# Kernel tuning notes

Measured on AMD Instinct MI355X. Metric: run time of the kernel, lower is better.

The kernel has to match this reference:

```python
import jax, jax.numpy as jnp
import numpy as np

N_NODES = 50000
N_EDGES = 800000
IN_FEATS = 128
OUT_FEATS = 128


def setup_inputs() -> dict:
    key = jax.random.key(0)
    k1, k2, k3, k4 = jax.random.split(key, 4)
    feature = jax.random.normal(k1, (N_NODES, IN_FEATS), dtype=jnp.float32)
    src = jax.random.randint(k2, (N_EDGES,), 0, N_NODES, dtype=jnp.int64)
    dst = jax.random.randint(k3, (N_EDGES,), 0, N_NODES, dtype=jnp.int64)
    # nn.Linear(in_feats, out_feats): W is [out, in], b is [out]
    bound = 1.0 / np.sqrt(IN_FEATS)
    W = jax.random.uniform(k4, (OUT_FEATS, IN_FEATS), minval=-bound, maxval=bound, dtype=jnp.float32)
    b = jnp.zeros((OUT_FEATS,), dtype=jnp.float32)
    return {"feature": feature, "src": src, "dst": dst, "W": W, "b": b}


def reference(feature, src, dst, W, b):
    # DGL update_all(copy_src('h'), sum('m','h')): h'[v] = sum over edges u->v of h[u]
    n_nodes = feature.shape[0]
    msgs = feature[src]  # [E, in_feats] gather
    agg = jax.ops.segment_sum(msgs, dst, num_segments=n_nodes)  # [N, in_feats]
    # linear: agg @ W.T + b
    return jnp.einsum("ni,oi->no", agg, W) + b
```

## Files before the change

kernel.cpp:

```cpp
#include <hip/hip_runtime.h>
#include <hip/hip_bf16.h>

#define N_FEATS 128
#define SCAN_CHUNK 1024

typedef __attribute__((ext_vector_type(8))) short bf16x8;
typedef __attribute__((ext_vector_type(4))) float f32x4;

__device__ __forceinline__ unsigned short f32_to_bf16_rne(float f) {
    unsigned u = __float_as_uint(f);
    u = u + 0x7FFFu + ((u >> 16) & 1u);
    return (unsigned short)(u >> 16);
}
__device__ __forceinline__ unsigned pack2(float a, float b) {
    return (unsigned)f32_to_bf16_rne(a) | ((unsigned)f32_to_bf16_rne(b) << 16);
}

__launch_bounds__(256)
__global__ void gcn_transform_mfma(const float* __restrict__ feat,
                                   const float* __restrict__ W,
                                   unsigned short* __restrict__ Y,
                                   int* __restrict__ deg, int n_nodes) {
    __shared__ unsigned short wlds[N_FEATS * N_FEATS];

    const int t = threadIdx.x;
    const long long gid = (long long)blockIdx.x * 256 + t;
    if (gid < n_nodes) deg[gid] = 0;

    {
        const int row = t >> 1;
        const int gbase = (t & 1) * 8;
        const float* wsrc = W + (size_t)row * N_FEATS + gbase * 8;
#pragma unroll
        for (int g = 0; g < 8; ++g) {
            float4 x0 = *reinterpret_cast<const float4*>(wsrc + g * 8);
            float4 x1 = *reinterpret_cast<const float4*>(wsrc + g * 8 + 4);
            uint4 q;
            q.x = pack2(x0.x, x0.y);
            q.y = pack2(x0.z, x0.w);
            q.z = pack2(x1.x, x1.y);
            q.w = pack2(x1.z, x1.w);
            int byte = row * 256 + (gbase + g) * 16;
            byte ^= (row & 7) << 4;
            *reinterpret_cast<uint4*>(reinterpret_cast<char*>(wlds) + byte) = q;
        }
    }
    __syncthreads();

    const int row0 = (blockIdx.x * 4 + (t >> 6)) * 16;
    if (row0 >= n_nodes) return;
    const int l = t & 63;
    const int lr = l & 15;
    const int kb = l >> 4;

    bf16x8 afrag[4] = {};
    if (row0 + lr < n_nodes) {
        const float* aptr = feat + (size_t)(row0 + lr) * N_FEATS + kb * 8;
#pragma unroll
        for (int kk = 0; kk < 4; ++kk) {
            float4 x0 = *reinterpret_cast<const float4*>(aptr + kk * 32);
            float4 x1 = *reinterpret_cast<const float4*>(aptr + kk * 32 + 4);
            bf16x8 af;
            af[0] = (short)f32_to_bf16_rne(x0.x);
            af[1] = (short)f32_to_bf16_rne(x0.y);
            af[2] = (short)f32_to_bf16_rne(x0.z);
            af[3] = (short)f32_to_bf16_rne(x0.w);
            af[4] = (short)f32_to_bf16_rne(x1.x);
            af[5] = (short)f32_to_bf16_rne(x1.y);
            af[6] = (short)f32_to_bf16_rne(x1.z);
            af[7] = (short)f32_to_bf16_rne(x1.w);
            afrag[kk] = af;
        }
    }

    f32x4 acc[8];
#pragma unroll
    for (int nt = 0; nt < 8; ++nt) acc[nt] = (f32x4){0.f, 0.f, 0.f, 0.f};

#pragma unroll
    for (int nt = 0; nt < 8; ++nt) {
        const int brow = nt * 16 + lr;
        const int swz = (brow & 7) << 4;
#pragma unroll
        for (int kk = 0; kk < 4; ++kk) {
            int byte = brow * 256 + (kk * 4 + kb) * 16;
            byte ^= swz;
            bf16x8 bfrag = *reinterpret_cast<const bf16x8*>(
                reinterpret_cast<const char*>(wlds) + byte);
            acc[nt] = __builtin_amdgcn_mfma_f32_16x16x32_bf16(afrag[kk], bfrag, acc[nt], 0, 0, 0);
        }
    }

#pragma unroll
    for (int nt = 0; nt < 8; ++nt) {
        const int col = nt * 16 + lr;
#pragma unroll
        for (int j = 0; j < 4; ++j) {
            const int r = row0 + kb * 4 + j;
            if (r < n_nodes)
                Y[(size_t)r * N_FEATS + col] = f32_to_bf16_rne(acc[nt][j]);
        }
    }
}

__global__ void gcn_hist_pos(const int* __restrict__ src, const int* __restrict__ dst,
                             int* __restrict__ deg, int* __restrict__ pos,
                             int n_edges, int n_nodes) {
    int e = blockIdx.x * blockDim.x + threadIdx.x;
    if (e >= n_edges) return;
    int d = dst[e];
    int s = src[e];
    if ((unsigned)d < (unsigned)n_nodes && (unsigned)s < (unsigned)n_nodes)
        pos[e] = atomicAdd(&deg[d], 1);
}

__launch_bounds__(256)
__global__ void gcn_scan(const int* __restrict__ deg, int* __restrict__ row_start,
                         int n, int nchunks) {
    const int t = threadIdx.x;
    const int b = blockIdx.x;
    const int base = b * SCAN_CHUNK;

    int v = 0;
    for (int j = t; j < base; j += 256) v += deg[j];
    for (int d = 1; d < 64; d <<= 1) v += __shfl_xor(v, d, 64);
    __shared__ int owsum[4];
    __shared__ int s_off;
    if ((t & 63) == 0) owsum[t >> 6] = v;
    __syncthreads();
    if (t == 0) s_off = owsum[0] + owsum[1] + owsum[2] + owsum[3];
    __syncthreads();
    const int chunk_off = s_off;

    const int idx0 = base + t * 4;
    int x[4];
#pragma unroll
    for (int k = 0; k < 4; ++k) {
        int idx = idx0 + k;
        x[k] = (idx < n) ? deg[idx] : 0;
    }
    const int tsum = x[0] + x[1] + x[2] + x[3];

    const int lane = t & 63, w = t >> 6;
    int inc = tsum;
    for (int d = 1; d < 64; d <<= 1) {
        int sv = __shfl_up(inc, d, 64);
        if (lane >= d) inc += sv;
    }
    __shared__ int wsum[4];
    if (lane == 63) wsum[w] = inc;
    __syncthreads();
    int woff = 0;
    for (int i = 0; i < w; ++i) woff += wsum[i];

    int run = chunk_off + woff + inc - tsum;
#pragma unroll
    for (int k = 0; k < 4; ++k) {
        int idx = idx0 + k;
        if (idx < n) row_start[idx] = run;
        run += x[k];
    }

    if (t == 0 && b == nchunks - 1)
        row_start[n] = chunk_off + wsum[0] + wsum[1] + wsum[2] + wsum[3];
}

__global__ void gcn_build_csr_pos(const int* __restrict__ src, const int* __restrict__ dst,
                                  const int* __restrict__ row_start, const int* __restrict__ pos,
                                  int* __restrict__ csr_src, int n_edges, int n_nodes) {
    int e = blockIdx.x * blockDim.x + threadIdx.x;
    if (e >= n_edges) return;
    int d = dst[e];
    int s = src[e];
    if ((unsigned)d >= (unsigned)n_nodes || (unsigned)s >= (unsigned)n_nodes) return;
    csr_src[row_start[d] + pos[e]] = s;
}

#define BACC(acc, v)                                              \
    do {                                                          \
        unsigned uu;                                              \
        uu = (v).x;                                               \
        acc[0] += __uint_as_float(uu << 16);                      \
        acc[1] += __uint_as_float(uu & 0xFFFF0000u);              \
        uu = (v).y;                                               \
        acc[2] += __uint_as_float(uu << 16);                      \
        acc[3] += __uint_as_float(uu & 0xFFFF0000u);              \
        uu = (v).z;                                               \
        acc[4] += __uint_as_float(uu << 16);                      \
        acc[5] += __uint_as_float(uu & 0xFFFF0000u);              \
        uu = (v).w;                                               \
        acc[6] += __uint_as_float(uu << 16);                      \
        acc[7] += __uint_as_float(uu & 0xFFFF0000u);              \
    } while (0)

__launch_bounds__(256)
__global__ void gcn_aggregate_half(const uint4* __restrict__ Y,
                                   const int* __restrict__ row_start,
                                   const int* __restrict__ csr_src,
                                   const float* __restrict__ bias,
                                   float* __restrict__ out, int n_nodes) {
    const int wid = blockIdx.x * 4 + (threadIdx.x >> 6);
    const int half = (wid >= n_nodes) ? 1 : 0;
    const int node = wid - half * n_nodes;
    if (node >= n_nodes) return;
    const int l = threadIdx.x & 63;
    const int g = l >> 3;
    const int ql = l & 7;
    const int beg = row_start[node];
    const int end = row_start[node + 1];
    const int coff = half * 8 + ql;

    float a0[8] = {0,0,0,0,0,0,0,0};
    float a1[8] = {0,0,0,0,0,0,0,0};

    int i = beg;
    for (; i + 16 <= end; i += 16) {
        int s0 = csr_src[i + g];
        int s1 = csr_src[i + 8 + g];
        uint4 v0 = Y[(size_t)s0 * 16 + coff];
        uint4 v1 = Y[(size_t)s1 * 16 + coff];
        BACC(a0, v0);
        BACC(a1, v1);
    }
    if (i + 8 <= end) {
        int s0 = csr_src[i + g];
        uint4 v0 = Y[(size_t)s0 * 16 + coff];
        BACC(a0, v0);
        i += 8;
    }
    int rem = end - i;
    if (g < rem) {
        int s0 = csr_src[i + g];
        uint4 v0 = Y[(size_t)s0 * 16 + coff];
        BACC(a0, v0);
    }

    float r[8];
#pragma unroll
    for (int k = 0; k < 8; ++k) {
        r[k] = a0[k] + a1[k];
        r[k] += __shfl_xor(r[k], 8, 64);
        r[k] += __shfl_xor(r[k], 16, 64);
        r[k] += __shfl_xor(r[k], 32, 64);
    }

    if (g == 0) {
        const int cbase = half * 64 + ql * 8;
        const float4 b0 = *reinterpret_cast<const float4*>(bias + cbase);
        const float4 b1 = *reinterpret_cast<const float4*>(bias + cbase + 4);
        float4* o4 = reinterpret_cast<float4*>(out + (size_t)node * N_FEATS + cbase);
        o4[0] = make_float4(r[0] + b0.x, r[1] + b0.y, r[2] + b0.z, r[3] + b0.w);
        o4[1] = make_float4(r[4] + b1.x, r[5] + b1.y, r[6] + b1.z, r[7] + b1.w);
    }
}

__global__ void gcn_init_c(const float* __restrict__ W, float* __restrict__ Wt) {
    int t = blockIdx.x * blockDim.x + threadIdx.x;
    if (t < N_FEATS * N_FEATS) {
        int o = t >> 7;
        int i = t & 127;
        Wt[i * N_FEATS + o] = W[o * N_FEATS + i];
    }
}

__global__ void gcn_scatter_add(const float* __restrict__ feat,
                                const int* __restrict__ src,
                                const int* __restrict__ dst,
                                float* __restrict__ agg,
                                int n_edges, int n_nodes) {
    long long tid = (long long)blockIdx.x * blockDim.x + threadIdx.x;
    int e = (int)(tid >> 5);
    if (e >= n_edges) return;
    int j = (int)(tid & 31);
    int s = src[e];
    int d = dst[e];
    if ((unsigned)s >= (unsigned)n_nodes || (unsigned)d >= (unsigned)n_nodes) return;
    const float4 v = *reinterpret_cast<const float4*>(feat + (size_t)s * N_FEATS + j * 4);
    float* p = agg + (size_t)d * N_FEATS + j * 4;
    atomicAdd(p + 0, v.x);
    atomicAdd(p + 1, v.y);
    atomicAdd(p + 2, v.z);
    atomicAdd(p + 3, v.w);
}

__launch_bounds__(256)
__global__ void gcn_gemm_inplace(float* __restrict__ out,
                                 const float* __restrict__ Wt,
                                 const float* __restrict__ b,
                                 int n_nodes) {
    __shared__ float a_lds[32 * N_FEATS];

    const int t = threadIdx.x;
    const int node0 = blockIdx.x * 32;
    const int rows = min(32, n_nodes - node0);

    float4* a4 = reinterpret_cast<float4*>(a_lds);
    const float4* out4 = reinterpret_cast<const float4*>(out + (size_t)node0 * N_FEATS);
    const int nflt4 = rows * (N_FEATS / 4);
    for (int idx = t; idx < nflt4; idx += 256) a4[idx] = out4[idx];
    __syncthreads();

    const int oq = t & 31;
    const int ng = t >> 5;

    const float4 bb = reinterpret_cast<const float4*>(b)[oq];
    float4 acc[4];
#pragma unroll
    for (int k = 0; k < 4; ++k) acc[k] = bb;

    const float4* Wt4 = reinterpret_cast<const float4*>(Wt);
#pragma unroll 4
    for (int i = 0; i < N_FEATS; ++i) {
        const float4 w = Wt4[i * 32 + oq];
#pragma unroll
        for (int k = 0; k < 4; ++k) {
            const float a = a_lds[(ng * 4 + k) * N_FEATS + i];
            acc[k].x += a * w.x;
            acc[k].y += a * w.y;
            acc[k].z += a * w.z;
            acc[k].w += a * w.w;
        }
    }

    __syncthreads();

#pragma unroll
    for (int k = 0; k < 4; ++k) {
        const int r = ng * 4 + k;
        if (r < rows) {
            reinterpret_cast<float4*>(out + (size_t)(node0 + r) * N_FEATS)[oq] = acc[k];
        }
    }
}

extern "C" void kernel_launch(void* const* d_in, const int* in_sizes, int n_in,
                              void* d_out, int out_size, void* d_ws, size_t ws_size,
                              hipStream_t stream) {
    const float* feature = (const float*)d_in[0];
    const int*   src     = (const int*)d_in[1];
    const int*   dst     = (const int*)d_in[2];
    const float* W       = (const float*)d_in[3];
    const float* b       = (const float*)d_in[4];
    float* out = (float*)d_out;

    const int n_nodes = in_sizes[0] / N_FEATS;
    const int n_edges = in_sizes[1];
    const int nchunks = (n_nodes + SCAN_CHUNK - 1) / SCAN_CHUNK;

    char* ws = (char*)d_ws;
    size_t off = 0;
    auto take = [&](size_t bytes) -> char* {
        char* p = ws + off;
        off = (off + bytes + 255) & ~(size_t)255;
        return p;
    };
    int* deg       = (int*)take((size_t)n_nodes * sizeof(int));
    int* row_start = (int*)take(((size_t)n_nodes + 1) * sizeof(int));
    int* csr_src   = (int*)take((size_t)n_edges * sizeof(int));
    unsigned short* Yb = (unsigned short*)take((size_t)n_nodes * N_FEATS * sizeof(unsigned short));
    int* pos       = (int*)take((size_t)n_edges * sizeof(int));
    const bool tierA2 = (off <= ws_size);

    if (tierA2) {
        gcn_transform_mfma<<<(n_nodes + 63) / 64, 256, 0, stream>>>(
            feature, W, Yb, deg, n_nodes);
        const int eblocks = (n_edges + 255) / 256;
        gcn_hist_pos<<<eblocks, 256, 0, stream>>>(src, dst, deg, pos, n_edges, n_nodes);
        gcn_scan<<<nchunks, 256, 0, stream>>>(deg, row_start, n_nodes, nchunks);
        gcn_build_csr_pos<<<eblocks, 256, 0, stream>>>(
            src, dst, row_start, pos, csr_src, n_edges, n_nodes);
        const int nwaves = 2 * n_nodes;
        gcn_aggregate_half<<<(nwaves + 3) / 4, 256, 0, stream>>>(
            reinterpret_cast<const uint4*>(Yb), row_start, csr_src, b, out, n_nodes);
    } else {
        float* Wt = (float*)d_ws;
        gcn_init_c<<<(N_FEATS * N_FEATS + 255) / 256, 256, 0, stream>>>(W, Wt);
        hipMemsetAsync(d_out, 0, (size_t)n_nodes * N_FEATS * sizeof(float), stream);
        long long total = (long long)n_edges * 32;
        gcn_scatter_add<<<(int)((total + 255) / 256), 256, 0, stream>>>(
            feature, src, dst, out, n_edges, n_nodes);
        gcn_gemm_inplace<<<(n_nodes + 31) / 32, 256, 0, stream>>>(out, Wt, b, n_nodes);
    }
}
```

Measured before the change: 137.8 us.

## Precompute bf16 W once and read from global; one wave per node aggregation

Adds a small init kernel that converts W to bf16 once and zeroes the degree array, so the MFMA transform kernel no longer restages a 32KB swizzled LDS copy of W in every block and instead reads B fragments straight from global memory (likely served from cache). The aggregation kernel changes from two waves per node, each handling half the features, to one wave per node covering all 128 features, with four edges processed per step and four accumulator sets. This removes redundant per-block W conversion and halves the number of row_start reads per node. In exchange it adds a kernel launch and relies on cache hits for the B reads, and the aggregation uses more registers per wave with less edge-level parallelism.

```diff
diff --git a/kernel.cpp b/kernel.cpp
--- a/kernel.cpp
+++ b/kernel.cpp
@@ -12,44 +12,36 @@
     u = u + 0x7FFFu + ((u >> 16) & 1u);
     return (unsigned short)(u >> 16);
 }
-__device__ __forceinline__ unsigned pack2(float a, float b) {
-    return (unsigned)f32_to_bf16_rne(a) | ((unsigned)f32_to_bf16_rne(b) << 16);
+
+__global__ void gcn_init(const float* __restrict__ W, unsigned short* __restrict__ Wb,
+                         int* __restrict__ deg, int n_nodes) {
+    int t = blockIdx.x * blockDim.x + threadIdx.x;
+    if (t < N_FEATS * N_FEATS / 8) {
+        const float4* f4 = reinterpret_cast<const float4*>(W) + (size_t)t * 2;
+        float4 x0 = f4[0];
+        float4 x1 = f4[1];
+        ushort4 o0, o1;
+        o0.x = f32_to_bf16_rne(x0.x); o0.y = f32_to_bf16_rne(x0.y);
+        o0.z = f32_to_bf16_rne(x0.z); o0.w = f32_to_bf16_rne(x0.w);
+        o1.x = f32_to_bf16_rne(x1.x); o1.y = f32_to_bf16_rne(x1.y);
+        o1.z = f32_to_bf16_rne(x1.z); o1.w = f32_to_bf16_rne(x1.w);
+        reinterpret_cast<ushort4*>(Wb)[(size_t)t * 2 + 0] = o0;
+        reinterpret_cast<ushort4*>(Wb)[(size_t)t * 2 + 1] = o1;
+    }
+    int u = t - N_FEATS * N_FEATS / 8;
+    if (u >= 0 && u < n_nodes) deg[u] = 0;
 }
 
 __launch_bounds__(256)
 __global__ void gcn_transform_mfma(const float* __restrict__ feat,
-                                   const float* __restrict__ W,
+                                   const unsigned short* __restrict__ Wb,
                                    unsigned short* __restrict__ Y,
-                                   int* __restrict__ deg, int n_nodes) {
-    __shared__ unsigned short wlds[N_FEATS * N_FEATS];
-
-    const int t = threadIdx.x;
-    const long long gid = (long long)blockIdx.x * 256 + t;
-    if (gid < n_nodes) deg[gid] = 0;
-
-    {
-        const int row = t >> 1;
-        const int gbase = (t & 1) * 8;
-        const float* wsrc = W + (size_t)row * N_FEATS + gbase * 8;
-#pragma unroll
-        for (int g = 0; g < 8; ++g) {
-            float4 x0 = *reinterpret_cast<const float4*>(wsrc + g * 8);
-            float4 x1 = *reinterpret_cast<const float4*>(wsrc + g * 8 + 4);
-            uint4 q;
-            q.x = pack2(x0.x, x0.y);
-            q.y = pack2(x0.z, x0.w);
-            q.z = pack2(x1.x, x1.y);
-            q.w = pack2(x1.z, x1.w);
-            int byte = row * 256 + (gbase + g) * 16;
-            byte ^= (row & 7) << 4;
-            *reinterpret_cast<uint4*>(reinterpret_cast<char*>(wlds) + byte) = q;
-        }
-    }
-    __syncthreads();
-
-    const int row0 = (blockIdx.x * 4 + (t >> 6)) * 16;
+                                   int n_nodes) {
+    const long long gtid = (long long)blockIdx.x * blockDim.x + threadIdx.x;
+    const int wave = (int)(gtid >> 6);
+    const int row0 = wave * 16;
     if (row0 >= n_nodes) return;
-    const int l = t & 63;
+    const int l = (int)(threadIdx.x & 63);
     const int lr = l & 15;
     const int kb = l >> 4;
 
@@ -79,14 +71,10 @@
 
 #pragma unroll
     for (int nt = 0; nt < 8; ++nt) {
-        const int brow = nt * 16 + lr;
-        const int swz = (brow & 7) << 4;
+        const unsigned short* wp = Wb + (size_t)(nt * 16 + lr) * N_FEATS + kb * 8;
 #pragma unroll
         for (int kk = 0; kk < 4; ++kk) {
-            int byte = brow * 256 + (kk * 4 + kb) * 16;
-            byte ^= swz;
-            bf16x8 bfrag = *reinterpret_cast<const bf16x8*>(
-                reinterpret_cast<const char*>(wlds) + byte);
+            bf16x8 bfrag = *reinterpret_cast<const bf16x8*>(wp + kk * 32);
             acc[nt] = __builtin_amdgcn_mfma_f32_16x16x32_bf16(afrag[kk], bfrag, acc[nt], 0, 0, 0);
         }
     }
@@ -194,61 +182,63 @@
     } while (0)
 
 __launch_bounds__(256)
-__global__ void gcn_aggregate_half(const uint4* __restrict__ Y,
+__global__ void gcn_aggregate_bf16(const uint4* __restrict__ Y,
                                    const int* __restrict__ row_start,
                                    const int* __restrict__ csr_src,
                                    const float* __restrict__ bias,
                                    float* __restrict__ out, int n_nodes) {
-    const int wid = blockIdx.x * 4 + (threadIdx.x >> 6);
-    const int half = (wid >= n_nodes) ? 1 : 0;
-    const int node = wid - half * n_nodes;
+    int node = blockIdx.x * 4 + (threadIdx.x >> 6);
     if (node >= n_nodes) return;
     const int l = threadIdx.x & 63;
-    const int g = l >> 3;
-    const int ql = l & 7;
-    const int beg = row_start[node];
-    const int end = row_start[node + 1];
-    const int coff = half * 8 + ql;
+    const int qw = l >> 4;
+    const int ql = l & 15;
+    int beg = row_start[node];
+    int end = row_start[node + 1];
 
     float a0[8] = {0,0,0,0,0,0,0,0};
     float a1[8] = {0,0,0,0,0,0,0,0};
+    float a2[8] = {0,0,0,0,0,0,0,0};
+    float a3[8] = {0,0,0,0,0,0,0,0};
 
     int i = beg;
     for (; i + 16 <= end; i += 16) {
-        int s0 = csr_src[i + g];
-        int s1 = csr_src[i + 8 + g];
-        uint4 v0 = Y[(size_t)s0 * 16 + coff];
-        uint4 v1 = Y[(size_t)s1 * 16 + coff];
+        int s0 = csr_src[i + qw];
+        int s1 = csr_src[i + 4 + qw];
+        int s2 = csr_src[i + 8 + qw];
+        int s3 = csr_src[i + 12 + qw];
+        uint4 v0 = Y[(size_t)s0 * 16 + ql];
+        uint4 v1 = Y[(size_t)s1 * 16 + ql];
+        uint4 v2 = Y[(size_t)s2 * 16 + ql];
+        uint4 v3 = Y[(size_t)s3 * 16 + ql];
         BACC(a0, v0);
         BACC(a1, v1);
-    }
-    if (i + 8 <= end) {
-        int s0 = csr_src[i + g];
-        uint4 v0 = Y[(size_t)s0 * 16 + coff];
-        BACC(a0, v0);
-        i += 8;
+        BACC(a2, v2);
+        BACC(a3, v3);
+    }
+    for (; i + 4 <= end; i += 4) {
+        int s = csr_src[i + qw];
+        uint4 v = Y[(size_t)s * 16 + ql];
+        BACC(a0, v);
     }
     int rem = end - i;
-    if (g < rem) {
-        int s0 = csr_src[i + g];
-        uint4 v0 = Y[(size_t)s0 * 16 + coff];
-        BACC(a0, v0);
+    if (qw < rem) {
+        int s = csr_src[i + qw];
+        uint4 v = Y[(size_t)s * 16 + ql];
+        BACC(a0, v);
     }
 
     float r[8];
 #pragma unroll
     for (int k = 0; k < 8; ++k) {
-        r[k] = a0[k] + a1[k];
-        r[k] += __shfl_xor(r[k], 8, 64);
+        r[k] = a0[k] + a1[k] + a2[k] + a3[k];
         r[k] += __shfl_xor(r[k], 16, 64);
         r[k] += __shfl_xor(r[k], 32, 64);
     }
 
-    if (g == 0) {
-        const int cbase = half * 64 + ql * 8;
-        const float4 b0 = *reinterpret_cast<const float4*>(bias + cbase);
-        const float4 b1 = *reinterpret_cast<const float4*>(bias + cbase + 4);
-        float4* o4 = reinterpret_cast<float4*>(out + (size_t)node * N_FEATS + cbase);
+    if (qw == 0) {
+        const float4 b0 = *reinterpret_cast<const float4*>(bias + ql * 8);
+        const float4 b1 = *reinterpret_cast<const float4*>(bias + ql * 8 + 4);
+        float4* o4 = reinterpret_cast<float4*>(out + (size_t)node * N_FEATS + ql * 8);
         o4[0] = make_float4(r[0] + b0.x, r[1] + b0.y, r[2] + b0.z, r[3] + b0.w);
         o4[1] = make_float4(r[4] + b1.x, r[5] + b1.y, r[6] + b1.z, r[7] + b1.w);
     }
@@ -358,19 +348,22 @@
     int* row_start = (int*)take(((size_t)n_nodes + 1) * sizeof(int));
     int* csr_src   = (int*)take((size_t)n_edges * sizeof(int));
     unsigned short* Yb = (unsigned short*)take((size_t)n_nodes * N_FEATS * sizeof(unsigned short));
+    unsigned short* Wb = (unsigned short*)take((size_t)N_FEATS * N_FEATS * sizeof(unsigned short));
     int* pos       = (int*)take((size_t)n_edges * sizeof(int));
     const bool tierA2 = (off <= ws_size);
 
     if (tierA2) {
-        gcn_transform_mfma<<<(n_nodes + 63) / 64, 256, 0, stream>>>(
-            feature, W, Yb, deg, n_nodes);
+        const int init_elems = N_FEATS * N_FEATS / 8 + n_nodes;
+        gcn_init<<<(init_elems + 255) / 256, 256, 0, stream>>>(W, Wb, deg, n_nodes);
+        const long long nthr = (long long)((n_nodes + 15) / 16) * 64;
+        gcn_transform_mfma<<<(int)((nthr + 255) / 256), 256, 0, stream>>>(
+            feature, Wb, Yb, n_nodes);
         const int eblocks = (n_edges + 255) / 256;
         gcn_hist_pos<<<eblocks, 256, 0, stream>>>(src, dst, deg, pos, n_edges, n_nodes);
         gcn_scan<<<nchunks, 256, 0, stream>>>(deg, row_start, n_nodes, nchunks);
         gcn_build_csr_pos<<<eblocks, 256, 0, stream>>>(
             src, dst, row_start, pos, csr_src, n_edges, n_nodes);
-        const int nwaves = 2 * n_nodes;
-        gcn_aggregate_half<<<(nwaves + 3) / 4, 256, 0, stream>>>(
+        gcn_aggregate_bf16<<<(n_nodes + 3) / 4, 256, 0, stream>>>(
             reinterpret_cast<const uint4*>(Yb), row_start, csr_src, b, out, n_nodes);
     } else {
         float* Wt = (float*)d_ws;
```

Result: slower. 145.2 us (+5.4%).
